# Kernel optimization log

Hardware: AMD Instinct MI355X
Metric: run time of the kernel (lower is better)

Reference implementation:

```python
import math
import jax, jax.numpy as jnp
import numpy as np

B, N, QN, LN = 2, 2048, 512, 256
D, QD, LD = 1024, 1024, 64
H, QH = 16, 16
HD, QHD = D // H, QD // QH


def setup_inputs() -> dict:
    key = jax.random.key(0)
    ks = jax.random.split(key, 12)
    g = lambda k, shp, s: (jax.random.normal(k, shp, dtype=jnp.float32) * s)
    return {
        "x": g(ks[0], (B, N, D), 1.0),
        "query": g(ks[1], (B, QN, QD), 1.0),
        "low_res": g(ks[2], (B, LN, LD), 1.0),
        "W_qkv": g(ks[3], (D, 3 * D), 0.02),          # self.qkv (no bias)
        "W_xkv": g(ks[4], (D, 2 * QD), 0.02),         # self.x_to_query_kv
        "W_qlin": g(ks[5], (QD, 3 * QD), 0.02),       # self.query_linear
        "gate": g(ks[6], (1, QH, 1, 1), 0.5),         # self.gate
        "W_proj": g(ks[7], (D, D), 0.02),
        "b_proj": jnp.zeros((D,), jnp.float32),
        "W_qproj": g(ks[8], (QD, QD), 0.02),
        "b_qproj": jnp.zeros((QD,), jnp.float32),
        "W_lrproj": g(ks[9], (LD, LD), 0.02),
        "b_lrproj": jnp.zeros((LD,), jnp.float32),
    }


def _sdpa(q, k, v):
    # q,k,v: [B, H, S, hd]; plain softmax attention, no mask, no dropout
    scale = 1.0 / math.sqrt(q.shape[-1])
    attn = jax.nn.softmax(jnp.einsum("bhqd,bhkd->bhqk", q, k) * scale, axis=-1)
    return jnp.einsum("bhqk,bhkd->bhqd", attn, v)


def reference(x, query, low_res, W_qkv, W_xkv, W_qlin, gate,
              W_proj, b_proj, W_qproj, b_qproj, W_lrproj, b_lrproj):
    # --- self-attention over x ---
    qkv = (x @ W_qkv).reshape(B, N, 3, H, HD).transpose(2, 0, 3, 1, 4)
    q, k, v = qkv[0], qkv[1], qkv[2]          # [B,H,N,HD]
    x_attn = _sdpa(q, k, v)                    # [B,H,N,HD]

    # --- zero_init gated cross-attention for query stream ---
    kv = (x @ W_xkv).reshape(B, N, 2, QH, QHD).transpose(2, 0, 3, 1, 4)
    k2, v2 = kv[0], kv[1]                      # [B,QH,N,QHD]
    qqkv = (query @ W_qlin).reshape(B, QN, 3, QH, QHD).transpose(2, 0, 3, 1, 4)
    qq, qk, qv = qqkv[0], qqkv[1], qqkv[2]     # [B,QH,QN,QHD]

    xk = jnp.concatenate([k2, qk], axis=2)     # [B,QH,N+QN,QHD]
    xv = jnp.concatenate([v2, qv], axis=2)
    scale = 1.0 / math.sqrt(QHD)
    scores = jnp.einsum("bhqd,bhkd->bhqk", qq, xk) * scale  # [B,QH,QN,N+QN]
    # split softmax with learned tanh gate on the x segment
    attn = jnp.concatenate(
        [jnp.tanh(gate) * jax.nn.softmax(scores[..., :N], axis=-1),
         jax.nn.softmax(scores[..., N:], axis=-1)], axis=-1)
    q_attn = jnp.einsum("bhqk,bhkd->bhqd", attn, xv)  # [B,QH,QN,QHD]

    # --- output projections ---
    x_out = x_attn.transpose(0, 2, 1, 3).reshape(B, N, D) @ W_proj + b_proj
    query_out = q_attn.transpose(0, 2, 1, 3).reshape(B, QN, QD) @ W_qproj + b_qproj
    # faithful to source: low_res passes through unmodified in zero_init branch,
    # then transpose(1,2)+reshape scramble, then proj
    lr_out = jnp.swapaxes(low_res, 1, 2).reshape(B, LN, LD) @ W_lrproj + b_lrproj
    return (x_out, query_out, lr_out)
```

## Files before the change

### kernel.cpp

```cpp
#include <hip/hip_runtime.h>

typedef __bf16 bf16;
typedef __bf16 bf16x4 __attribute__((ext_vector_type(4)));
typedef __bf16 bf16x8 __attribute__((ext_vector_type(8)));
typedef float  f32x4  __attribute__((ext_vector_type(4)));


#define AS1(p) ((const __attribute__((address_space(1))) void*)(p))
#define AS3(p) ((__attribute__((address_space(3))) void*)(p))
__device__ __forceinline__ void gl16(const void* g, void* l) {
    __builtin_amdgcn_global_load_lds(AS1(g), AS3(l), 16, 0, 0);
}
#define BAR_VM4() asm volatile("s_waitcnt vmcnt(4)\n\ts_barrier" ::: "memory")
#define BAR_VM2() asm volatile("s_waitcnt vmcnt(2)\n\ts_barrier" ::: "memory")
#define BAR_VM0() asm volatile("s_waitcnt vmcnt(0)\n\ts_barrier" ::: "memory")
#define BAR()     asm volatile("s_barrier" ::: "memory")

__global__ __launch_bounds__(256) void prep(
    const float* __restrict__ x, bf16* __restrict__ xb,
    const float* __restrict__ query, bf16* __restrict__ qryb,
    const float* __restrict__ W_qkv, const float* __restrict__ W_xkv,
    const float* __restrict__ W_qlin, const float* __restrict__ W_proj,
    const float* __restrict__ W_qproj,
    bf16* __restrict__ WtX, bf16* __restrict__ Wtqlin,
    bf16* __restrict__ Wtproj, bf16* __restrict__ Wtqproj,
    const float* __restrict__ lowres, const float* __restrict__ W_lr,
    const float* __restrict__ b_lr, float* __restrict__ lrout)
{
    __shared__ float T[64][65];
    const int bid = blockIdx.x, tid = threadIdx.x;

    if (bid < 2560) {
        int idx = (bid * 256 + tid) << 3;
        const float* s; bf16* d;
        if (idx < 4194304) { s = x + idx; d = xb + idx; }
        else { int k = idx - 4194304; s = query + k; d = qryb + k; }
        f32x4 a = *(const f32x4*)s, c = *(const f32x4*)(s + 4);
        bf16x8 v;
#pragma unroll
        for (int j = 0; j < 4; j++) { v[j] = (bf16)a[j]; v[4 + j] = (bf16)c[j]; }
        *(bf16x8*)d = v;
    } else if (bid < 5120) {
        int w = bid - 2560;
        int gx = w % 160, k0 = (w / 160) << 6;
        const float* S; bf16* D; int N;
        if (gx < 48)       { S = W_qkv;   D = WtX;     N = 3072; }
        else if (gx < 80)  { S = W_xkv;   D = WtX + (size_t)3072 * 1024; N = 2048; gx -= 48; }
        else if (gx < 128) { S = W_qlin;  D = Wtqlin;  N = 3072; gx -= 80; }
        else if (gx < 144) { S = W_proj;  D = Wtproj;  N = 1024; gx -= 128; }
        else               { S = W_qproj; D = Wtqproj; N = 1024; gx -= 144; }
        int n0 = gx << 6;
#pragma unroll
        for (int rr = 0; rr < 4; rr++) {
            int row = (rr << 4) + (tid >> 4), col = (tid & 15) << 2;
            f32x4 v = *(const f32x4*)(S + (size_t)(k0 + row) * N + n0 + col);
#pragma unroll
            for (int j = 0; j < 4; j++) T[col + j][row] = v[j];
        }
        __syncthreads();
        {
            int n = tid >> 2, kc = (tid & 3) << 4;
            bf16x8 v0, v1;
#pragma unroll
            for (int j = 0; j < 8; j++) {
                v0[j] = (bf16)T[n][kc + j];
                v1[j] = (bf16)T[n][kc + 8 + j];
            }
            bf16* dp = D + (size_t)(n0 + n) * 1024 + k0 + kc;
            *(bf16x8*)dp = v0; *(bf16x8*)(dp + 8) = v1;
        }
    } else {
        int idx = (bid - 5120) * 256 + tid;
        int j = idx & 63, i = (idx >> 6) & 255, b = idx >> 14;
        float acc = b_lr[j];
        const float* lr = lowres + ((size_t)b << 14);
        for (int k = 0; k < 64; k++) {
            int f = i * 64 + k;
            acc += lr[((f & 255) << 6) + (f >> 8)] * W_lr[(k << 6) + j];
        }
        lrout[idx] = acc;
    }
}

template <int NSPLIT, typename OT>
__device__ __forceinline__ void gemm_core(
    bf16* gsm,
    const bf16* __restrict__ A, const bf16* __restrict__ Bt,
    OT* __restrict__ C0, OT* __restrict__ C1, OT* __restrict__ C2,
    OT* __restrict__ C3, OT* __restrict__ C4,
    const float* __restrict__ bias, int N, int K, int tshift,
    float s0scale, unsigned vmask, int bx, int by)
{
    const int tid  = threadIdx.x;
    const int wave = tid >> 6, lane = tid & 63;
    const int l15  = lane & 15, g = lane >> 4;
    const int wr   = wave & 1, wc = wave >> 1;
    const int m0   = by << 7, n0 = bx << 7;

    f32x4 acc[4][4] = {};

    auto stage = [&](int t, int bsel) {
        const bf16* Ab = A  + (size_t)m0 * K + (t << 5);
        const bf16* Bb = Bt + (size_t)n0 * K + (t << 5);
        char* Ad = (char*)gsm + (bsel << 14);
        char* Bd = Ad + 8192;
        const int wb = (tid & 192) << 4;
#pragma unroll
        for (int i = 0; i < 2; i++) {
            int L = (i << 8) + tid;
            int r = L >> 2, c = (L & 3) ^ ((r ^ (r >> 2)) & 3);
            gl16(Ab + (size_t)r * K + (c << 3), Ad + (i << 12) + wb);
            gl16(Bb + (size_t)r * K + (c << 3), Bd + (i << 12) + wb);
        }
    };
    auto compute = [&](int bsel) {
        const char* Ad = (const char*)gsm + (bsel << 14);
        const char* Bd = Ad + 8192;
        bf16x8 af[4], bq[4];
#pragma unroll
        for (int mb = 0; mb < 4; mb++) {
            int row = (wr << 6) + (mb << 4) + l15;
            af[mb] = *(const bf16x8*)(Ad + (row << 6)
                      + ((g ^ ((row ^ (row >> 2)) & 3)) << 4));
        }
#pragma unroll
        for (int nb = 0; nb < 4; nb++) {
            int row = (wc << 6) + (nb << 4) + l15;
            bq[nb] = *(const bf16x8*)(Bd + (row << 6)
                      + ((g ^ ((row ^ (row >> 2)) & 3)) << 4));
        }
#pragma unroll
        for (int mb = 0; mb < 4; mb++)
#pragma unroll
            for (int nb = 0; nb < 4; nb++)
                acc[mb][nb] = __builtin_amdgcn_mfma_f32_16x16x32_bf16(
                    af[mb], bq[nb], acc[mb][nb], 0, 0, 0);
    };

    const int T = K >> 5;
    stage(0, 0);
    for (int t = 0; t < T; t++) {
        int bsel = t & 1;
        if (t + 1 < T) { stage(t + 1, bsel ^ 1); BAR_VM4(); }
        else           { BAR_VM0(); }
        compute(bsel);
        BAR();
    }

    if constexpr (NSPLIT == 0) {
#pragma unroll
        for (int mb = 0; mb < 4; mb++)
#pragma unroll
            for (int nb = 0; nb < 4; nb++) {
                int n = n0 + (wc << 6) + (nb << 4) + l15;
                int mbase = m0 + (wr << 6) + (mb << 4) + (g << 2);
                float bi = bias[n];
#pragma unroll
                for (int r = 0; r < 4; r++)
                    C0[(size_t)(mbase + r) * N + n] = (OT)(acc[mb][nb][r] + bi);
            }
    } else {
        BAR();
        bf16* stg = gsm + wave * 4608;
        const int nh = (n0 >> 6) + wc;
        const int sl = nh >> 4, hq = nh & 15;
        const float scl = (sl == 0) ? s0scale : 1.0f;
        const bool isv = (vmask >> sl) & 1;
        if (isv) {
#pragma unroll
            for (int mb = 0; mb < 4; mb++)
#pragma unroll
                for (int nb = 0; nb < 4; nb++)
#pragma unroll
                    for (int r = 0; r < 4; r++)
                        stg[((nb << 4) + l15) * 72 + (mb << 4) + (g << 2) + r]
                            = (bf16)(acc[mb][nb][r] * scl);
        } else {
#pragma unroll
            for (int mb = 0; mb < 4; mb++)
#pragma unroll
                for (int nb = 0; nb < 4; nb++)
#pragma unroll
                    for (int r = 0; r < 4; r++)
                        stg[((mb << 4) + (g << 2) + r) << 6 | ((nb << 4) + l15)]
                            = (bf16)(acc[mb][nb][r] * scl);
        }
        __syncthreads();
        const int ntok = 1 << tshift;
        const int tok0 = m0 + (wr << 6);
        const int b = tok0 >> tshift, t0 = tok0 & (ntok - 1);
        const int bh_ = (b << 4) + hq;
        OT* dst = (sl == 0) ? C0 : (sl == 1) ? C1 : (sl == 2) ? C2
                : (sl == 3) ? C3 : C4;
#pragma unroll
        for (int rr = 0; rr < 8; rr++) {
            int idx = (rr << 6) + lane;
            int rowi = idx >> 3, c = idx & 7;
            if (isv) {
                bf16x8 vv = *(const bf16x8*)&stg[rowi * 72 + (c << 3)];
                bf16x4 lo, hi;
#pragma unroll
                for (int jj = 0; jj < 4; jj++) { lo[jj] = vv[jj]; hi[jj] = vv[4 + jj]; }
                int tb = t0 + ((c >> 2) << 5);
                int gamma0 = (c << 1) & 7;
                int p_lo = (((gamma0 & 3) << 1) + (gamma0 >> 2)) << 2;
                size_t base = ((size_t)((bh_ << 6) + rowi)) * ntok + tb;
                *(bf16x4*)&dst[base + p_lo] = lo;
                *(bf16x4*)&dst[base + p_lo + 8] = hi;
            } else {
                bf16x8 vv = *(const bf16x8*)&stg[(rowi << 6) + (c << 3)];
                *(bf16x8*)&dst[(((size_t)bh_ * ntok + t0 + rowi) << 6) + (c << 3)] = vv;
            }
        }
    }
}

__global__ __launch_bounds__(256) void gemm_qkv(
    const bf16* __restrict__ A0, const bf16* __restrict__ Bt0,
    bf16* __restrict__ qb, bf16* __restrict__ kb, bf16* __restrict__ vbt,
    bf16* __restrict__ k2, bf16* __restrict__ v2t,
    const bf16* __restrict__ A1, const bf16* __restrict__ Bt1,
    bf16* __restrict__ qq, bf16* __restrict__ qk, bf16* __restrict__ qvt,
    float sc2)
{
    __shared__ __align__(16) bf16 gsm[18432];
    int idx = (blockIdx.x & 7) * 184 + (blockIdx.x >> 3);
    const bf16 *A, *Bt; bf16 *C0, *C1, *C2, *C3, *C4;
    int N, tshift, bx, by; unsigned vmask;
    if (idx < 1280) {
        A = A0; Bt = Bt0; C0 = qb; C1 = kb; C2 = vbt; C3 = k2; C4 = v2t;
        N = 5120; tshift = 11; vmask = 0b10100u; bx = idx % 40; by = idx / 40;
    } else {
        idx -= 1280;
        A = A1; Bt = Bt1; C0 = qq; C1 = qk; C2 = qvt; C3 = nullptr; C4 = nullptr;
        N = 3072; tshift = 9; vmask = 0b100u; bx = idx % 24; by = idx / 24;
    }
    gemm_core<1, bf16>(gsm, A, Bt, C0, C1, C2, C3, C4, nullptr,
                       N, 1024, tshift, sc2, vmask, bx, by);
}

__global__ __launch_bounds__(256) void gemm_proj(
    const bf16* __restrict__ ax, const bf16* __restrict__ Wtp,
    float* __restrict__ o0, const float* __restrict__ bp,
    const bf16* __restrict__ aq, const bf16* __restrict__ Wtq,
    float* __restrict__ o1, const float* __restrict__ bq)
{
    __shared__ __align__(16) bf16 gsm[18432];
    int idx = (blockIdx.x & 7) * 40 + (blockIdx.x >> 3);
    const bf16 *A, *Bt; float* C; const float* bias; int bx, by;
    if (idx < 256) { A = ax; Bt = Wtp; C = o0; bias = bp; bx = idx & 7; by = idx >> 3; }
    else { idx -= 256; A = aq; Bt = Wtq; C = o1; bias = bq; bx = idx & 7; by = idx >> 3; }
    gemm_core<0, float>(gsm, A, Bt, C, nullptr, nullptr, nullptr, nullptr, bias,
                        1024, 1024, 0, 1.0f, 0u, bx, by);
}

__global__ __launch_bounds__(256) void flash3m(
    const bf16* __restrict__ Q1, const bf16* __restrict__ K1,
    const bf16* __restrict__ V1t, bf16* __restrict__ O1,
    const bf16* __restrict__ Q2, const bf16* __restrict__ K2a,
    const bf16* __restrict__ V2at, const bf16* __restrict__ K2b,
    const bf16* __restrict__ V2bt, bf16* __restrict__ O2,
    const float* __restrict__ gate)
{
    __shared__ __align__(16) bf16 fsm[8704];

    const int tid = threadIdx.x;
    const int wave = tid >> 6, lane = tid & 63;
    const int l15 = lane & 15, g = lane >> 4;

    const int j = blockIdx.x & 7, i = blockIdx.x >> 3;
    const bf16 *Qp, *Ka, *Vat, *Kb2, *Vbt2; bf16* Op;
    int nq, nk1, nk2, q0, bh;
    bool cross;
    if (i < 16) {
        cross = true;
        bh = (j << 2) + (i >> 2); q0 = (i & 3) << 7;
        Qp = Q2; Ka = K2a; Vat = V2at; Kb2 = K2b; Vbt2 = V2bt; Op = O2;
        nq = 512; nk1 = 2048; nk2 = 512;
    } else {
        cross = false;
        int is = i - 16;
        bh = (j << 2) + (is >> 4); q0 = (is & 15) << 7;
        Qp = Q1; Ka = K1; Vat = V1t; Kb2 = nullptr; Vbt2 = nullptr; Op = O1;
        nq = 2048; nk1 = 2048; nk2 = 0;
    }
    const int h = bh & 15, b = bh >> 4;
    const int T1 = nk1 >> 5, T = T1 + (cross ? (nk2 >> 5) : 0);

    bf16x8 qf[2][2];
#pragma unroll
    for (int qb = 0; qb < 2; qb++) {
        const bf16* qrow = Qp + ((size_t)bh * nq + q0 + (wave << 5) + (qb << 4) + l15) * 64;
        qf[qb][0] = *(const bf16x8*)(qrow + (g << 3));
        qf[qb][1] = *(const bf16x8*)(qrow + 32 + (g << 3));
    }

    bf16x8 ones;
#pragma unroll
    for (int z = 0; z < 8; z++) ones[z] = (bf16)1.0f;

    f32x4 Oacc[4][2] = {}, Ofin[4][2] = {};
    f32x4 Lones[2] = {};
    const float gmul = cross ? tanhf(gate[h]) : 1.0f;

    const int kr = tid >> 3, kc = (tid & 7) ^ (kr & 7);
    const int vr = tid >> 2, vc = (tid & 3) ^ (vr & 3);
    const bf16* kaddr = Ka + ((size_t)bh * nk1) * 64 + (kr << 6) + (kc << 3);
    const bf16* vaddr = Vat + ((size_t)bh << 6) * nk1 + (size_t)vr * nk1 + (vc << 3);
    int staged = 0;

    auto stage = [&](int bsel) {
        if (cross && staged == T1) {
            kaddr = Kb2 + ((size_t)bh * nk2) * 64 + (kr << 6) + (kc << 3);
            vaddr = Vbt2 + ((size_t)bh << 6) * nk2 + (size_t)vr * nk2 + (vc << 3);
        }
        char* Kd = (char*)fsm + (bsel << 12);
        char* Vd = (char*)fsm + 8192 + (bsel << 12);
        const int wb = (tid & 192) << 4;
        gl16(kaddr, Kd + wb);
        gl16(vaddr, Vd + wb);
        kaddr += 2048;
        vaddr += 32;
        staged++;
    };

    auto compute = [&](int t, int bsel) {
        const char* Kb = (const char*)fsm + (bsel << 12);
        const char* Vb = (const char*)fsm + 8192 + (bsel << 12);
        f32x4 S[2][2];
#pragma unroll
        for (int nb = 0; nb < 2; nb++) {
            int row = (nb << 4) + l15;
            bf16x8 kf0 = *(const bf16x8*)(Kb + (row << 7) + ((g ^ (row & 7)) << 4));
            bf16x8 kf1 = *(const bf16x8*)(Kb + (row << 7) + (((4 + g) ^ (row & 7)) << 4));
#pragma unroll
            for (int qb = 0; qb < 2; qb++) {
                f32x4 s = {};
                s = __builtin_amdgcn_mfma_f32_16x16x32_bf16(kf0, qf[qb][0], s, 0, 0, 0);
                s = __builtin_amdgcn_mfma_f32_16x16x32_bf16(kf1, qf[qb][1], s, 0, 0, 0);
                S[nb][qb] = s;
            }
        }
        bf16x8 pf[2];
#pragma unroll
        for (int qb = 0; qb < 2; qb++)
#pragma unroll
            for (int r = 0; r < 4; r++) {
                pf[qb][r]     = (bf16)__builtin_amdgcn_exp2f(S[0][qb][r]);
                pf[qb][4 + r] = (bf16)__builtin_amdgcn_exp2f(S[1][qb][r]);
            }
#pragma unroll
        for (int qb = 0; qb < 2; qb++)
            Lones[qb] = __builtin_amdgcn_mfma_f32_16x16x32_bf16(
                ones, pf[qb], Lones[qb], 0, 0, 0);
#pragma unroll
        for (int hb = 0; hb < 4; hb++) {
            int row = (hb << 4) + l15;
            bf16x8 vf = *(const bf16x8*)(Vb + (row << 6) + ((g ^ (row & 3)) << 4));
#pragma unroll
            for (int qb = 0; qb < 2; qb++)
                Oacc[hb][qb] = __builtin_amdgcn_mfma_f32_16x16x32_bf16(
                    vf, pf[qb], Oacc[hb][qb], 0, 0, 0);
        }
        if (cross && t == T1 - 1) {
#pragma unroll
            for (int qb = 0; qb < 2; qb++) {
                float w = gmul / Lones[qb][0];
#pragma unroll
                for (int hb = 0; hb < 4; hb++)
#pragma unroll
                    for (int r = 0; r < 4; r++) {
                        Ofin[hb][qb][r] += Oacc[hb][qb][r] * w;
                        Oacc[hb][qb][r] = 0.0f;
                    }
                Lones[qb] = f32x4{};
            }
        }
    };

    stage(0);
    for (int t = 0; t < T; t++) {
        int bsel = t & 1;
        if (t + 1 < T) { stage(bsel ^ 1); BAR_VM2(); }
        else           { BAR_VM0(); }
        compute(t, bsel);
        BAR();
    }

    float wfin[2];
#pragma unroll
    for (int qb = 0; qb < 2; qb++)
        wfin[qb] = (cross ? 1.0f : gmul) / Lones[qb][0];

    bf16* OB = fsm;
#pragma unroll
    for (int hb = 0; hb < 4; hb++)
#pragma unroll
        for (int qb = 0; qb < 2; qb++)
#pragma unroll
            for (int r = 0; r < 4; r++) {
                float v = Oacc[hb][qb][r] * wfin[qb];
                if (cross) v += Ofin[hb][qb][r];
                OB[((hb << 4) + (g << 2) + r) * 136 + (wave << 5) + (qb << 4) + l15] = (bf16)v;
            }
    __syncthreads();
    {
        int q = tid >> 1, half = (tid & 1) << 5;
        bf16x8 o[4];
#pragma unroll
        for (int j2 = 0; j2 < 4; j2++)
#pragma unroll
            for (int jj = 0; jj < 8; jj++)
                o[j2][jj] = OB[(half + (j2 << 3) + jj) * 136 + q];
        bf16* op = Op + (((size_t)b * nq + q0 + q) << 10) + (h << 6) + half;
#pragma unroll
        for (int j2 = 0; j2 < 4; j2++)
            *(bf16x8*)(op + (j2 << 3)) = o[j2];
    }
}

extern "C" void kernel_launch(void* const* d_in, const int* in_sizes, int n_in,
                              void* d_out, int out_size, void* d_ws, size_t ws_size,
                              hipStream_t stream)
{
    const float* x       = (const float*)d_in[0];
    const float* query   = (const float*)d_in[1];
    const float* lowres  = (const float*)d_in[2];
    const float* W_qkv   = (const float*)d_in[3];
    const float* W_xkv   = (const float*)d_in[4];
    const float* W_qlin  = (const float*)d_in[5];
    const float* gate    = (const float*)d_in[6];
    const float* W_proj  = (const float*)d_in[7];
    const float* b_proj  = (const float*)d_in[8];
    const float* W_qproj = (const float*)d_in[9];
    const float* b_qproj = (const float*)d_in[10];
    const float* W_lr    = (const float*)d_in[11];
    const float* b_lr    = (const float*)d_in[12];
    float* out = (float*)d_out;

    const float sc2 = 0.125f * 1.44269504088896f;

    char* ws = (char*)d_ws;
    bf16* WtX     = (bf16*)ws; ws += 10485760;
    bf16* Wtqlin  = (bf16*)ws; ws += 6291456;
    bf16* Wtproj  = (bf16*)ws; ws += 2097152;
    bf16* Wtqproj = (bf16*)ws; ws += 2097152;
    bf16* xb      = (bf16*)ws; ws += 8388608;
    bf16* qryb    = (bf16*)ws; ws += 2097152;
    bf16* qb      = (bf16*)ws; ws += 8388608;
    bf16* kb      = (bf16*)ws; ws += 8388608;
    bf16* vbt     = (bf16*)ws; ws += 8388608;
    bf16* k2      = (bf16*)ws; ws += 8388608;
    bf16* v2t     = (bf16*)ws; ws += 8388608;
    bf16* qq      = (bf16*)ws; ws += 2097152;
    bf16* qk      = (bf16*)ws; ws += 2097152;
    bf16* qvt     = (bf16*)ws; ws += 2097152;
    bf16* ax = xb;
    bf16* aq = qryb;

    prep<<<5248, 256, 0, stream>>>(
        x, xb, query, qryb, W_qkv, W_xkv, W_qlin, W_proj, W_qproj,
        WtX, Wtqlin, Wtproj, Wtqproj, lowres, W_lr, b_lr, out + 5242880);

    gemm_qkv<<<1472, 256, 0, stream>>>(
        xb, WtX, qb, kb, vbt, k2, v2t, qryb, Wtqlin, qq, qk, qvt, sc2);

    flash3m<<<640, 256, 0, stream>>>(
        qb, kb, vbt, ax, qq, k2, v2t, qk, qvt, aq, gate);

    gemm_proj<<<320, 256, 0, stream>>>(
        ax, Wtproj, out, b_proj, aq, Wtqproj, out + 4194304, b_qproj);

    (void)in_sizes; (void)n_in; (void)out_size; (void)ws_size;
}
```

Before: 285.6 us.

## Double flash attention KV tile to 64 keys and remap QKV GEMM blocks per XCD

The flash attention kernel now stages 64 keys per iteration instead of 32, doubling the LDS buffers and issuing four async loads per stage. This halves the number of barrier and wait rounds per attention block and gives more MFMA work between synchronisations. The QKV GEMM block index mapping is also rearranged so each XCD gets a contiguous patch of output tiles, which should improve L2 reuse of A and B panels. In exchange the kernel uses more LDS and more registers, which may lower occupancy.

```diff
diff --git a/kernel.cpp b/kernel.cpp
--- a/kernel.cpp
+++ b/kernel.cpp
@@ -12,7 +12,6 @@
     __builtin_amdgcn_global_load_lds(AS1(g), AS3(l), 16, 0, 0);
 }
 #define BAR_VM4() asm volatile("s_waitcnt vmcnt(4)\n\ts_barrier" ::: "memory")
-#define BAR_VM2() asm volatile("s_waitcnt vmcnt(2)\n\ts_barrier" ::: "memory")
 #define BAR_VM0() asm volatile("s_waitcnt vmcnt(0)\n\ts_barrier" ::: "memory")
 #define BAR()     asm volatile("s_barrier" ::: "memory")
 
@@ -224,16 +223,18 @@
     float sc2)
 {
     __shared__ __align__(16) bf16 gsm[18432];
-    int idx = (blockIdx.x & 7) * 184 + (blockIdx.x >> 3);
+    const int xcd = blockIdx.x & 7, s = blockIdx.x >> 3;
     const bf16 *A, *Bt; bf16 *C0, *C1, *C2, *C3, *C4;
     int N, tshift, bx, by; unsigned vmask;
-    if (idx < 1280) {
+    if (s < 160) {
+        int k = s / 20, w = s % 20;
+        by = (k << 2) + w / 5; bx = xcd * 5 + w % 5;
         A = A0; Bt = Bt0; C0 = qb; C1 = kb; C2 = vbt; C3 = k2; C4 = v2t;
-        N = 5120; tshift = 11; vmask = 0b10100u; bx = idx % 40; by = idx / 40;
+        N = 5120; tshift = 11; vmask = 0b10100u;
     } else {
-        idx -= 1280;
+        by = xcd; bx = s - 160;
         A = A1; Bt = Bt1; C0 = qq; C1 = qk; C2 = qvt; C3 = nullptr; C4 = nullptr;
-        N = 3072; tshift = 9; vmask = 0b100u; bx = idx % 24; by = idx / 24;
+        N = 3072; tshift = 9; vmask = 0b100u;
     }
     gemm_core<1, bf16>(gsm, A, Bt, C0, C1, C2, C3, C4, nullptr,
                        N, 1024, tshift, sc2, vmask, bx, by);
@@ -262,7 +263,7 @@
     const bf16* __restrict__ V2bt, bf16* __restrict__ O2,
     const float* __restrict__ gate)
 {
-    __shared__ __align__(16) bf16 fsm[8704];
+    __shared__ __align__(16) bf16 fsm[16384];
 
     const int tid = threadIdx.x;
     const int wave = tid >> 6, lane = tid & 63;
@@ -285,7 +286,7 @@
         nq = 2048; nk1 = 2048; nk2 = 0;
     }
     const int h = bh & 15, b = bh >> 4;
-    const int T1 = nk1 >> 5, T = T1 + (cross ? (nk2 >> 5) : 0);
+    const int T1 = nk1 >> 6, T = T1 + (cross ? (nk2 >> 6) : 0);
 
     bf16x8 qf[2][2];
 #pragma unroll
@@ -303,33 +304,39 @@
     f32x4 Lones[2] = {};
     const float gmul = cross ? tanhf(gate[h]) : 1.0f;
 
-    const int kr = tid >> 3, kc = (tid & 7) ^ (kr & 7);
-    const int vr = tid >> 2, vc = (tid & 3) ^ (vr & 3);
-    const bf16* kaddr = Ka + ((size_t)bh * nk1) * 64 + (kr << 6) + (kc << 3);
-    const bf16* vaddr = Vat + ((size_t)bh << 6) * nk1 + (size_t)vr * nk1 + (vc << 3);
+    const int kr0 = tid >> 3, kc0 = (tid & 7) ^ (kr0 & 7);
+    const int kr1 = 32 + kr0, kc1 = (tid & 7) ^ (kr1 & 7);
+    const int koff0 = (kr0 << 6) + (kc0 << 3);
+    const int koff1 = (kr1 << 6) + (kc1 << 3);
+    const bf16* kaddr = Ka + (size_t)bh * nk1 * 64;
+    const bf16* va0 = Vat + ((size_t)bh << 6) * nk1 + (size_t)kr0 * nk1 + (kc0 << 3);
+    const bf16* va1 = Vat + ((size_t)bh << 6) * nk1 + (size_t)kr1 * nk1 + (kc1 << 3);
     int staged = 0;
 
     auto stage = [&](int bsel) {
         if (cross && staged == T1) {
-            kaddr = Kb2 + ((size_t)bh * nk2) * 64 + (kr << 6) + (kc << 3);
-            vaddr = Vbt2 + ((size_t)bh << 6) * nk2 + (size_t)vr * nk2 + (vc << 3);
-        }
-        char* Kd = (char*)fsm + (bsel << 12);
-        char* Vd = (char*)fsm + 8192 + (bsel << 12);
+            kaddr = Kb2 + (size_t)bh * nk2 * 64;
+            va0 = Vbt2 + ((size_t)bh << 6) * nk2 + (size_t)kr0 * nk2 + (kc0 << 3);
+            va1 = Vbt2 + ((size_t)bh << 6) * nk2 + (size_t)kr1 * nk2 + (kc1 << 3);
+        }
+        char* Kd = (char*)fsm + (bsel << 13);
+        char* Vd = (char*)fsm + 16384 + (bsel << 13);
         const int wb = (tid & 192) << 4;
-        gl16(kaddr, Kd + wb);
-        gl16(vaddr, Vd + wb);
-        kaddr += 2048;
-        vaddr += 32;
+        gl16(kaddr + koff0, Kd + wb);
+        gl16(va0,           Vd + wb);
+        gl16(kaddr + koff1, Kd + 4096 + wb);
+        gl16(va1,           Vd + 4096 + wb);
+        kaddr += 4096;
+        va0 += 64; va1 += 64;
         staged++;
     };
 
     auto compute = [&](int t, int bsel) {
-        const char* Kb = (const char*)fsm + (bsel << 12);
-        const char* Vb = (const char*)fsm + 8192 + (bsel << 12);
-        f32x4 S[2][2];
-#pragma unroll
-        for (int nb = 0; nb < 2; nb++) {
+        const char* Kb = (const char*)fsm + (bsel << 13);
+        const char* Vb = (const char*)fsm + 16384 + (bsel << 13);
+        f32x4 S[4][2];
+#pragma unroll
+        for (int nb = 0; nb < 4; nb++) {
             int row = (nb << 4) + l15;
             bf16x8 kf0 = *(const bf16x8*)(Kb + (row << 7) + ((g ^ (row & 7)) << 4));
             bf16x8 kf1 = *(const bf16x8*)(Kb + (row << 7) + (((4 + g) ^ (row & 7)) << 4));
@@ -341,26 +348,35 @@
                 S[nb][qb] = s;
             }
         }
-        bf16x8 pf[2];
+        bf16x8 pf[2][2];
 #pragma unroll
         for (int qb = 0; qb < 2; qb++)
 #pragma unroll
             for (int r = 0; r < 4; r++) {
-                pf[qb][r]     = (bf16)__builtin_amdgcn_exp2f(S[0][qb][r]);
-                pf[qb][4 + r] = (bf16)__builtin_amdgcn_exp2f(S[1][qb][r]);
-            }
-#pragma unroll
-        for (int qb = 0; qb < 2; qb++)
+                pf[qb][0][r]     = (bf16)__builtin_amdgcn_exp2f(S[0][qb][r]);
+                pf[qb][0][4 + r] = (bf16)__builtin_amdgcn_exp2f(S[1][qb][r]);
+                pf[qb][1][r]     = (bf16)__builtin_amdgcn_exp2f(S[2][qb][r]);
+                pf[qb][1][4 + r] = (bf16)__builtin_amdgcn_exp2f(S[3][qb][r]);
+            }
+#pragma unroll
+        for (int qb = 0; qb < 2; qb++) {
             Lones[qb] = __builtin_amdgcn_mfma_f32_16x16x32_bf16(
-                ones, pf[qb], Lones[qb], 0, 0, 0);
+                ones, pf[qb][0], Lones[qb], 0, 0, 0);
+            Lones[qb] = __builtin_amdgcn_mfma_f32_16x16x32_bf16(
+                ones, pf[qb][1], Lones[qb], 0, 0, 0);
+        }
 #pragma unroll
         for (int hb = 0; hb < 4; hb++) {
             int row = (hb << 4) + l15;
-            bf16x8 vf = *(const bf16x8*)(Vb + (row << 6) + ((g ^ (row & 3)) << 4));
-#pragma unroll
-            for (int qb = 0; qb < 2; qb++)
+            bf16x8 vf0 = *(const bf16x8*)(Vb + (row << 7) + ((g ^ (row & 7)) << 4));
+            bf16x8 vf1 = *(const bf16x8*)(Vb + (row << 7) + (((4 + g) ^ (row & 7)) << 4));
+#pragma unroll
+            for (int qb = 0; qb < 2; qb++) {
                 Oacc[hb][qb] = __builtin_amdgcn_mfma_f32_16x16x32_bf16(
-                    vf, pf[qb], Oacc[hb][qb], 0, 0, 0);
+                    vf0, pf[qb][0], Oacc[hb][qb], 0, 0, 0);
+                Oacc[hb][qb] = __builtin_amdgcn_mfma_f32_16x16x32_bf16(
+                    vf1, pf[qb][1], Oacc[hb][qb], 0, 0, 0);
+            }
         }
         if (cross && t == T1 - 1) {
 #pragma unroll
@@ -381,7 +397,7 @@
     stage(0);
     for (int t = 0; t < T; t++) {
         int bsel = t & 1;
-        if (t + 1 < T) { stage(bsel ^ 1); BAR_VM2(); }
+        if (t + 1 < T) { stage(bsel ^ 1); BAR_VM4(); }
         else           { BAR_VM0(); }
         compute(t, bsel);
         BAR();
```

New measurement: 290.6 us. Within noise of the previous version (+1.7%).
